# Optimization experiments

Measured on AMD Instinct MI355X. Metric: run time of the kernel, lower is better.

## Reference

```python
import jax, jax.numpy as jnp
import numpy as np

M = 0.25      # margin m
GAMMA = 64.0  # scale gamma
N, D = 8192, 128
NUM_CLASSES = 512


def setup_inputs() -> dict:
    key = jax.random.key(0)
    k1, k2 = jax.random.split(key)
    inputs = jax.random.normal(k1, (N, D), dtype=jnp.float32)
    targets = jax.random.randint(k2, (N,), 0, NUM_CLASSES, dtype=jnp.int64)
    return {"inputs": inputs, "targets": targets}


def reference(inputs, targets):
    # L2-normalize rows -> cosine similarity matrix [n, n]
    x = inputs / jnp.linalg.norm(inputs, axis=1, keepdims=True)
    sim = x @ x.T
    # positive mask: same label (includes diagonal, matching the torch code)
    mask = targets[:, None] == targets[None, :]

    Op, On = 1.0 + M, -M
    delta_p, delta_n = 1.0 - M, M

    sim_d = jax.lax.stop_gradient(sim)  # .detach() in torch
    ap = jnp.maximum(Op - sim_d, 0.0)
    an = jnp.maximum(sim_d + On, 0.0)

    logit_p = -ap * (sim - delta_p) * GAMMA
    logit_n = an * (sim - delta_n) * GAMMA

    neg_inf = jnp.float32(-jnp.inf)
    # per-row logsumexp over positives of -logit_p, over negatives of logit_n
    lp = jax.nn.logsumexp(jnp.where(mask, -logit_p, neg_inf), axis=1)
    ln = jax.nn.logsumexp(jnp.where(mask, neg_inf, logit_n), axis=1)

    return jnp.mean(jax.nn.softplus(ln + lp))
```

## Files before the change

kernel.cpp:

```cpp
#include <hip/hip_runtime.h>
#include <math.h>


#define NR    8192
#define DIMK  128
#define NT    64
#define NBLKS 512

typedef __attribute__((ext_vector_type(8))) short short8;
typedef __attribute__((ext_vector_type(4))) float f32x4;
typedef __attribute__((address_space(3))) uint32_t lds_u32;
typedef const __attribute__((address_space(1))) uint32_t glb_u32;

__device__ __forceinline__ unsigned short bf16_rne(float f) {
  uint32_t u = __float_as_uint(f);
  u += 0x7FFFu + ((u >> 16) & 1u);
  return (unsigned short)(u >> 16);
}


__global__ __launch_bounds__(256) void normalize_split_kernel(
    const float* __restrict__ x, unsigned short* __restrict__ xhi,
    unsigned short* __restrict__ xlo, float* __restrict__ gP,
    float* __restrict__ gN, int* __restrict__ counter) {
  if (blockIdx.x < 32)      gP[blockIdx.x * 256 + threadIdx.x] = 0.f;
  else if (blockIdx.x < 64) gN[(blockIdx.x - 32) * 256 + threadIdx.x] = 0.f;
  if (blockIdx.x == 64 && threadIdx.x == 0) *counter = 0;

  const int wave = threadIdx.x >> 6;
  const int lane = threadIdx.x & 63;
  const int row  = blockIdx.x * 4 + wave;
  const float2 v = ((const float2*)(x + (size_t)row * DIMK))[lane];
  float ss = v.x * v.x + v.y * v.y;
  #pragma unroll
  for (int s = 1; s < 64; s <<= 1) ss += __shfl_xor(ss, s);
  const float r = rsqrtf(ss);
  const float a = v.x * r, b = v.y * r;
  const unsigned short ha = bf16_rne(a), hb = bf16_rne(b);
  const float haf = __uint_as_float((uint32_t)ha << 16);
  const float hbf = __uint_as_float((uint32_t)hb << 16);
  ushort2 hi, lo;
  hi.x = ha; hi.y = hb;
  lo.x = bf16_rne(a - haf); lo.y = bf16_rne(b - hbf);
  ((ushort2*)xhi)[(size_t)row * 64 + lane] = hi;
  ((ushort2*)xlo)[(size_t)row * 64 + lane] = lo;
}

__global__ __launch_bounds__(512, 2) void simloss_kernel(
    const unsigned short* __restrict__ xhi, const unsigned short* __restrict__ xlo,
    const int* __restrict__ tgt, float* __restrict__ gP, float* __restrict__ gN,
    int* __restrict__ counter, float* __restrict__ out) {
  __shared__ unsigned short S[32768];
  __shared__ float colbuf[2][4][128][2];
  __shared__ int tAs[2][128];
  __shared__ int tBs[5][128];
  __shared__ float red[512];
  __shared__ int islast;

  const int tid  = threadIdx.x;
  const int wave = tid >> 6, lane = tid & 63;
  const int wy = wave & 3, wx = wave >> 2;
  const int q = lane >> 4, mcol = lane & 15;
  const bool isStage = (wy == 1) || (wy == 2);
  const bool isFlush = (wy == 0);
  const int srank = (wy - 1) + wx * 2;

  const int p  = blockIdx.x >> 4;
  const int b  = blockIdx.x & 15;
  const int n1 = NT - p;
  const int t0 = (b * (NT + 1)) >> 4;
  const int t1 = ((b + 1) * (NT + 1)) >> 4;
  const int ntile = t1 - t0;
  const int p2 = NT - 1 - p;

  int cur_bi = (t0 < n1) ? p : p2;

  if (tid < 128)       tAs[0][tid] = tgt[cur_bi * 128 + tid];
  else if (tid < 256)  tAs[1][tid - 128] = tgt[p2 * 128 + (tid - 128)];
  for (int v = tid; v < ntile * 128; v += 512) {
    const int ix = t0 + (v >> 7);
    const int bj = (ix < n1) ? p + ix : p2 + (ix - n1);
    tBs[v >> 7][v & 127] = tgt[bj * 128 + (v & 127)];
  }

  auto stageA = [&](int bi) {
    const unsigned short* gh = xhi + (size_t)bi * 128 * DIMK;
    const unsigned short* gl = xlo + (size_t)bi * 128 * DIMK;
    #pragma unroll
    for (int g = 0; g < 4; ++g) {
      const int r  = wave * 16 + g * 4 + (lane >> 4);
      const int sc = (lane & 15) ^ (r & 15);
      __builtin_amdgcn_global_load_lds((glb_u32*)(gh + (size_t)r * DIMK + sc * 8),
          (lds_u32*)&S[(wave * 16 + g * 4) * 128], 16, 0, 0);
      __builtin_amdgcn_global_load_lds((glb_u32*)(gl + (size_t)r * DIMK + sc * 8),
          (lds_u32*)&S[16384 + (wave * 16 + g * 4) * 128], 16, 0, 0);
    }
  };
  auto stageB = [&](int bj, int buf) {
    const unsigned short* gb = xhi + (size_t)bj * 128 * DIMK;
    unsigned short* dst = &S[buf * 16384];
    #pragma unroll
    for (int g = 0; g < 8; ++g) {
      const int r  = srank * 32 + g * 4 + (lane >> 4);
      const int sc = (lane & 15) ^ (r & 15);
      __builtin_amdgcn_global_load_lds((glb_u32*)(gb + (size_t)r * DIMK + sc * 8),
          (lds_u32*)&dst[(srank * 32 + g * 4) * 128], 16, 0, 0);
    }
  };

  short8 Ah[2][4], Al[2][4];
  int ta[2][4];
  auto extractA = [&](int seg) {
    #pragma unroll
    for (int fr = 0; fr < 2; ++fr) {
      const int r = wy * 32 + fr * 16 + mcol;
      #pragma unroll
      for (int ks = 0; ks < 4; ++ks) {
        const int pc = (ks * 4 + q) ^ mcol;
        Ah[fr][ks] = *(const short8*)&S[r * 128 + pc * 8];
        Al[fr][ks] = *(const short8*)&S[16384 + r * 128 + pc * 8];
      }
    }
    #pragma unroll
    for (int fr = 0; fr < 2; ++fr)
      #pragma unroll
      for (int rg = 0; rg < 4; ++rg)
        ta[fr][rg] = tAs[seg][wy * 32 + fr * 16 + q * 4 + rg];
  };

  float rowP[2][4] = {{0.f}}, rowN[2][4] = {{0.f}};
  auto flushRows = [&](int bi) {
    #pragma unroll
    for (int fr = 0; fr < 2; ++fr)
      #pragma unroll
      for (int rg = 0; rg < 4; ++rg) {
        float vp = rowP[fr][rg], vn = rowN[fr][rg];
        #pragma unroll
        for (int m = 1; m < 16; m <<= 1) {
          vp += __shfl_xor(vp, m);
          vn += __shfl_xor(vn, m);
        }
        if (mcol == 0) {
          const int row = bi * 128 + wy * 32 + fr * 16 + q * 4 + rg;
          atomicAdd(&gP[row], vp);
          atomicAdd(&gN[row], vn);
        }
      }
  };

  stageA(cur_bi);
  __syncthreads();
  extractA(0);
  __builtin_amdgcn_s_waitcnt(49279);
  __builtin_amdgcn_s_barrier();
  if (isStage) stageB((t0 < n1) ? p + t0 : p2 + (t0 - n1), 0);

  for (int tl = 0; tl < ntile; ++tl) {
    const int ix = t0 + tl;
    const int bi = (ix < n1) ? p : p2;
    const int bj = (ix < n1) ? p + ix : p2 + (ix - n1);

    if (bi != cur_bi) {
      flushRows(cur_bi);
      cur_bi = bi;
      stageA(cur_bi);
      __syncthreads();
      extractA(1);
      #pragma unroll
      for (int fr = 0; fr < 2; ++fr)
        #pragma unroll
        for (int rg = 0; rg < 4; ++rg) { rowP[fr][rg] = 0.f; rowN[fr][rg] = 0.f; }
      __builtin_amdgcn_s_waitcnt(49279);
      __builtin_amdgcn_s_barrier();
      if (isStage) stageB(bj, tl & 1);
    }

    if (isStage) __builtin_amdgcn_s_waitcnt(112);
    __builtin_amdgcn_s_barrier();

    if (tl + 1 < ntile) {
      const int ix2 = ix + 1;
      if ((ix2 < n1) == (ix < n1)) {
        const int bj2 = (ix2 < n1) ? p + ix2 : p2 + (ix2 - n1);
        if (isStage) stageB(bj2, (tl + 1) & 1);
      }
    }

    const unsigned short* Bb = &S[(tl & 1) * 16384];
    f32x4 acc[2][4];
    #pragma unroll
    for (int fr = 0; fr < 2; ++fr)
      #pragma unroll
      for (int fc = 0; fc < 4; ++fc)
        acc[fr][fc] = (f32x4){0.f, 0.f, 0.f, 0.f};
    #pragma unroll
    for (int ks = 0; ks < 4; ++ks) {
      short8 bh[4];
      #pragma unroll
      for (int fc = 0; fc < 4; ++fc) {
        const int rb = wx * 64 + fc * 16 + mcol;
        const int pc = (ks * 4 + q) ^ mcol;
        bh[fc] = *(const short8*)&Bb[rb * 128 + pc * 8];
      }
      #pragma unroll
      for (int fc = 0; fc < 4; ++fc) {
        acc[0][fc] = __builtin_amdgcn_mfma_f32_16x16x32_bf16(Ah[0][ks], bh[fc], acc[0][fc], 0, 0, 0);
        acc[1][fc] = __builtin_amdgcn_mfma_f32_16x16x32_bf16(Ah[1][ks], bh[fc], acc[1][fc], 0, 0, 0);
        acc[0][fc] = __builtin_amdgcn_mfma_f32_16x16x32_bf16(Al[0][ks], bh[fc], acc[0][fc], 0, 0, 0);
        acc[1][fc] = __builtin_amdgcn_mfma_f32_16x16x32_bf16(Al[1][ks], bh[fc], acc[1][fc], 0, 0, 0);
      }
    }

    int tb[4];
    #pragma unroll
    for (int fc = 0; fc < 4; ++fc) tb[fc] = tBs[tl][wx * 64 + fc * 16 + mcol];
    float cP[4] = {0.f, 0.f, 0.f, 0.f}, cN[4] = {0.f, 0.f, 0.f, 0.f};
    #pragma unroll
    for (int fr = 0; fr < 2; ++fr) {
      #pragma unroll
      for (int rg = 0; rg < 4; ++rg) {
        const int taa = ta[fr][rg];
        float vp = 0.f, vn = 0.f;
        #pragma unroll
        for (int fc = 0; fc < 4; ++fc) {
          const float s  = acc[fr][fc][rg];
          const bool pos = (taa == tb[fc]);
          const float ap = fmaxf(1.25f - s, 0.f);
          const float an = fmaxf(s - 0.25f, 0.f);
          const float arg = pos ? ap * fmaf(s, 64.f, -48.f) : an * an * 64.f;
          const float e = __expf(arg);
          const float ep = pos ? e : 0.f;
          const float en = pos ? 0.f : e;
          vp += ep; vn += en;
          cP[fc] += ep; cN[fc] += en;
        }
        rowP[fr][rg] += vp;
        rowN[fr][rg] += vn;
      }
    }

    #pragma unroll
    for (int fc = 0; fc < 4; ++fc) {
      cP[fc] += __shfl_xor(cP[fc], 16); cP[fc] += __shfl_xor(cP[fc], 32);
      cN[fc] += __shfl_xor(cN[fc], 16); cN[fc] += __shfl_xor(cN[fc], 32);
    }
    if (q == 0) {
      #pragma unroll
      for (int fc = 0; fc < 4; ++fc) {
        float2 v; v.x = cP[fc]; v.y = cN[fc];
        *(float2*)&colbuf[tl & 1][wy][wx * 64 + fc * 16 + mcol][0] = v;
      }
    }
    __builtin_amdgcn_s_waitcnt(49279);
    __builtin_amdgcn_s_barrier();

    if (isFlush && bj != bi) {
      const int col = wx * 64 + lane;
      float sp = 0.f, sn = 0.f;
      #pragma unroll
      for (int w = 0; w < 4; ++w) {
        const float2 v = *(const float2*)&colbuf[tl & 1][w][col][0];
        sp += v.x; sn += v.y;
      }
      atomicAdd(&gP[bj * 128 + col], sp);
      atomicAdd(&gN[bj * 128 + col], sn);
    }
  }
  flushRows(cur_bi);

  __builtin_amdgcn_s_waitcnt(0);
  __syncthreads();
  if (tid == 0) islast = (atomicAdd(counter, 1) == NBLKS - 1) ? 1 : 0;
  __syncthreads();
  if (islast) {
    float local = 0.f;
    #pragma unroll 1
    for (int bb = 0; bb < 2; ++bb) {
      const int base = bb * 4096 + tid * 8;
      float pv[8], nv[8];
      #pragma unroll
      for (int u = 0; u < 8; ++u) pv[u] = atomicAdd(&gP[base + u], 0.0f);
      #pragma unroll
      for (int u = 0; u < 8; ++u) nv[u] = atomicAdd(&gN[base + u], 0.0f);
      #pragma unroll
      for (int u = 0; u < 8; ++u) local += log1pf(pv[u] * nv[u]);
    }
    red[tid] = local;
    __syncthreads();
    for (int s2 = 256; s2 > 0; s2 >>= 1) {
      if (tid < s2) red[tid] += red[tid + s2];
      __syncthreads();
    }
    if (tid == 0) out[0] = red[0] / (float)NR;
  }
}

extern "C" void kernel_launch(void* const* d_in, const int* in_sizes, int n_in,
                              void* d_out, int out_size, void* d_ws, size_t ws_size,
                              hipStream_t stream) {
  const float* x  = (const float*)d_in[0];
  const int* tgt  = (const int*)d_in[1];
  float* out      = (float*)d_out;

  unsigned short* xhi = (unsigned short*)d_ws;
  unsigned short* xlo = xhi + (size_t)NR * DIMK;
  float* gP = (float*)((char*)d_ws + (size_t)NR * DIMK * 4);
  float* gN = gP + NR;
  int* counter = (int*)(gN + NR);

  normalize_split_kernel<<<NR / 4, 256, 0, stream>>>(x, xhi, xlo, gP, gN, counter);
  simloss_kernel<<<NBLKS, 512, 0, stream>>>(xhi, xlo, tgt, gP, gN, counter, out);
}
```

Baseline: 120.4 us.

## Treat all pairs as negatives and correct same-class pairs in a per-class pass

The main tiled loop now applies the negative-pair formula to every pair, with no label compares or selects. The exponent is rewritten as exp2 of a squared affine term using precomputed constants. The normalize kernel buckets row indices by class. Each block then handles one class: it computes that class's pairwise similarities in fp32, adds the positive terms and subtracts the negative terms that the main pass wrongly counted. This shrinks the per-element epilogue and drops the target staging, but adds a serial prologue, a memset launch, and a hard per-class cap (MAXC=120). Results are silently wrong if a class has more members than the cap, and the one-block-per-class mapping assumes the class count equals the block count.

```diff
diff --git a/kernel.cpp b/kernel.cpp
--- a/kernel.cpp
+++ b/kernel.cpp
@@ -6,6 +6,11 @@
 #define DIMK  128
 #define NT    64
 #define NBLKS 512
+#define NCLS  512
+#define MAXC  120
+
+#define CE1 9.6089795f
+#define CE0 -2.4022449f
 
 typedef __attribute__((ext_vector_type(8))) short short8;
 typedef __attribute__((ext_vector_type(4))) float f32x4;
@@ -18,11 +23,20 @@
   return (unsigned short)(u >> 16);
 }
 
+__device__ __forceinline__ float fexp2(float x) {
+#if __has_builtin(__builtin_amdgcn_exp2f)
+  return __builtin_amdgcn_exp2f(x);
+#else
+  return exp2f(x);
+#endif
+}
+
 
 __global__ __launch_bounds__(256) void normalize_split_kernel(
-    const float* __restrict__ x, unsigned short* __restrict__ xhi,
-    unsigned short* __restrict__ xlo, float* __restrict__ gP,
-    float* __restrict__ gN, int* __restrict__ counter) {
+    const float* __restrict__ x, const int* __restrict__ tgt,
+    unsigned short* __restrict__ xhi, unsigned short* __restrict__ xlo,
+    float* __restrict__ gP, float* __restrict__ gN,
+    int* __restrict__ cnt, int* __restrict__ idx, int* __restrict__ counter) {
   if (blockIdx.x < 32)      gP[blockIdx.x * 256 + threadIdx.x] = 0.f;
   else if (blockIdx.x < 64) gN[(blockIdx.x - 32) * 256 + threadIdx.x] = 0.f;
   if (blockIdx.x == 64 && threadIdx.x == 0) *counter = 0;
@@ -30,6 +44,13 @@
   const int wave = threadIdx.x >> 6;
   const int lane = threadIdx.x & 63;
   const int row  = blockIdx.x * 4 + wave;
+
+  if (lane == 0) {
+    const int t = tgt[row];
+    const int slot = atomicAdd(&cnt[t], 1);
+    if (slot < MAXC) idx[t * MAXC + slot] = row;
+  }
+
   const float2 v = ((const float2*)(x + (size_t)row * DIMK))[lane];
   float ss = v.x * v.x + v.y * v.y;
   #pragma unroll
@@ -48,13 +69,13 @@
 
 __global__ __launch_bounds__(512, 2) void simloss_kernel(
     const unsigned short* __restrict__ xhi, const unsigned short* __restrict__ xlo,
-    const int* __restrict__ tgt, float* __restrict__ gP, float* __restrict__ gN,
+    const int* __restrict__ cnt, const int* __restrict__ idx,
+    float* __restrict__ gP, float* __restrict__ gN,
     int* __restrict__ counter, float* __restrict__ out) {
   __shared__ unsigned short S[32768];
-  __shared__ float colbuf[2][4][128][2];
-  __shared__ int tAs[2][128];
-  __shared__ int tBs[5][128];
+  __shared__ float colbuf[2][4][128];
   __shared__ float red[512];
+  __shared__ int midx[MAXC];
   __shared__ int islast;
 
   const int tid  = threadIdx.x;
@@ -65,6 +86,38 @@
   const bool isFlush = (wy == 0);
   const int srank = (wy - 1) + wx * 2;
 
+  {
+    float* Sf = (float*)S;
+    const int cn = cnt[blockIdx.x];
+    const int m  = (cn < MAXC) ? cn : MAXC;
+    if (tid < m) midx[tid] = idx[blockIdx.x * MAXC + tid];
+    __syncthreads();
+    for (int v = tid; v < m * 128; v += 512) {
+      const int r = v >> 7, d = v & 127;
+      const int row = midx[r];
+      const float hi = __uint_as_float((uint32_t)xhi[(size_t)row * DIMK + d] << 16);
+      const float lo = __uint_as_float((uint32_t)xlo[(size_t)row * DIMK + d] << 16);
+      Sf[r * 129 + d] = hi + lo;
+    }
+    __syncthreads();
+    for (int pr = tid; pr < m * m; pr += 512) {
+      const int i = pr / m, j = pr - i * m;
+      const float* vi = &Sf[i * 129];
+      const float* vj = &Sf[j * 129];
+      float s = 0.f;
+      #pragma unroll 8
+      for (int d = 0; d < 128; ++d) s = fmaf(vi[d], vj[d], s);
+      const int gi = midx[i];
+      const float ep = __expf(fmaxf(1.25f - s, 0.f) * fmaf(s, 64.f, -48.f));
+      atomicAdd(&gP[gi], ep);
+      if (i != j) {
+        const float u = fmaxf(fmaf(s, CE1, CE0), 0.f);
+        atomicAdd(&gN[gi], -fexp2(u * u));
+      }
+    }
+    __syncthreads();
+  }
+
   const int p  = blockIdx.x >> 4;
   const int b  = blockIdx.x & 15;
   const int n1 = NT - p;
@@ -75,14 +128,6 @@
 
   int cur_bi = (t0 < n1) ? p : p2;
 
-  if (tid < 128)       tAs[0][tid] = tgt[cur_bi * 128 + tid];
-  else if (tid < 256)  tAs[1][tid - 128] = tgt[p2 * 128 + (tid - 128)];
-  for (int v = tid; v < ntile * 128; v += 512) {
-    const int ix = t0 + (v >> 7);
-    const int bj = (ix < n1) ? p + ix : p2 + (ix - n1);
-    tBs[v >> 7][v & 127] = tgt[bj * 128 + (v & 127)];
-  }
-
   auto stageA = [&](int bi) {
     const unsigned short* gh = xhi + (size_t)bi * 128 * DIMK;
     const unsigned short* gl = xlo + (size_t)bi * 128 * DIMK;
@@ -109,8 +154,7 @@
   };
 
   short8 Ah[2][4], Al[2][4];
-  int ta[2][4];
-  auto extractA = [&](int seg) {
+  auto extractA = [&]() {
     #pragma unroll
     for (int fr = 0; fr < 2; ++fr) {
       const int r = wy * 32 + fr * 16 + mcol;
@@ -121,36 +165,25 @@
         Al[fr][ks] = *(const short8*)&S[16384 + r * 128 + pc * 8];
       }
     }
+  };
+
+  float rowN[2][4] = {{0.f}};
+  auto flushRows = [&](int bi_) {
     #pragma unroll
     for (int fr = 0; fr < 2; ++fr)
       #pragma unroll
-      for (int rg = 0; rg < 4; ++rg)
-        ta[fr][rg] = tAs[seg][wy * 32 + fr * 16 + q * 4 + rg];
-  };
-
-  float rowP[2][4] = {{0.f}}, rowN[2][4] = {{0.f}};
-  auto flushRows = [&](int bi) {
-    #pragma unroll
-    for (int fr = 0; fr < 2; ++fr)
-      #pragma unroll
       for (int rg = 0; rg < 4; ++rg) {
-        float vp = rowP[fr][rg], vn = rowN[fr][rg];
+        float vn = rowN[fr][rg];
         #pragma unroll
-        for (int m = 1; m < 16; m <<= 1) {
-          vp += __shfl_xor(vp, m);
-          vn += __shfl_xor(vn, m);
-        }
-        if (mcol == 0) {
-          const int row = bi * 128 + wy * 32 + fr * 16 + q * 4 + rg;
-          atomicAdd(&gP[row], vp);
-          atomicAdd(&gN[row], vn);
-        }
+        for (int m2 = 1; m2 < 16; m2 <<= 1) vn += __shfl_xor(vn, m2);
+        if (mcol == 0)
+          atomicAdd(&gN[bi_ * 128 + wy * 32 + fr * 16 + q * 4 + rg], vn);
       }
   };
 
   stageA(cur_bi);
   __syncthreads();
-  extractA(0);
+  extractA();
   __builtin_amdgcn_s_waitcnt(49279);
   __builtin_amdgcn_s_barrier();
   if (isStage) stageB((t0 < n1) ? p + t0 : p2 + (t0 - n1), 0);
@@ -165,11 +198,11 @@
       cur_bi = bi;
       stageA(cur_bi);
       __syncthreads();
-      extractA(1);
+      extractA();
       #pragma unroll
       for (int fr = 0; fr < 2; ++fr)
         #pragma unroll
-        for (int rg = 0; rg < 4; ++rg) { rowP[fr][rg] = 0.f; rowN[fr][rg] = 0.f; }
+        for (int rg = 0; rg < 4; ++rg) rowN[fr][rg] = 0.f;
       __builtin_amdgcn_s_waitcnt(49279);
       __builtin_amdgcn_s_barrier();
       if (isStage) stageB(bj, tl & 1);
@@ -211,58 +244,52 @@
       }
     }
 
-    int tb[4];
-    #pragma unroll
-    for (int fc = 0; fc < 4; ++fc) tb[fc] = tBs[tl][wx * 64 + fc * 16 + mcol];
-    float cP[4] = {0.f, 0.f, 0.f, 0.f}, cN[4] = {0.f, 0.f, 0.f, 0.f};
-    #pragma unroll
-    for (int fr = 0; fr < 2; ++fr) {
-      #pragma unroll
-      for (int rg = 0; rg < 4; ++rg) {
-        const int taa = ta[fr][rg];
-        float vp = 0.f, vn = 0.f;
-        #pragma unroll
-        for (int fc = 0; fc < 4; ++fc) {
-          const float s  = acc[fr][fc][rg];
-          const bool pos = (taa == tb[fc]);
-          const float ap = fmaxf(1.25f - s, 0.f);
-          const float an = fmaxf(s - 0.25f, 0.f);
-          const float arg = pos ? ap * fmaf(s, 64.f, -48.f) : an * an * 64.f;
-          const float e = __expf(arg);
-          const float ep = pos ? e : 0.f;
-          const float en = pos ? 0.f : e;
-          vp += ep; vn += en;
-          cP[fc] += ep; cN[fc] += en;
-        }
-        rowP[fr][rg] += vp;
-        rowN[fr][rg] += vn;
-      }
-    }
+    float cN[4] = {0.f, 0.f, 0.f, 0.f};
+#define EPILOGUE(DIAG_)                                                      \
+    {                                                                        \
+      _Pragma("unroll")                                                      \
+      for (int fr = 0; fr < 2; ++fr) {                                       \
+        _Pragma("unroll")                                                    \
+        for (int rg = 0; rg < 4; ++rg) {                                     \
+          float vn = 0.f;                                                    \
+          _Pragma("unroll")                                                  \
+          for (int fc = 0; fc < 4; ++fc) {                                   \
+            const float s = acc[fr][fc][rg];                                 \
+            const float u = fmaxf(fmaf(s, CE1, CE0), 0.f);                   \
+            float e = fexp2(u * u);                                          \
+            if (DIAG_) {                                                     \
+              const int rl = wy * 32 + fr * 16 + q * 4 + rg;                 \
+              const int cl = wx * 64 + fc * 16 + mcol;                       \
+              e = (rl == cl) ? 0.f : e;                                      \
+            }                                                                \
+            vn += e;                                                         \
+            cN[fc] += e;                                                     \
+          }                                                                  \
+          rowN[fr][rg] += vn;                                                \
+        }                                                                    \
+      }                                                                      \
+    }
+    if (bj == bi) EPILOGUE(true) else EPILOGUE(false)
+#undef EPILOGUE
 
     #pragma unroll
     for (int fc = 0; fc < 4; ++fc) {
-      cP[fc] += __shfl_xor(cP[fc], 16); cP[fc] += __shfl_xor(cP[fc], 32);
-      cN[fc] += __shfl_xor(cN[fc], 16); cN[fc] += __shfl_xor(cN[fc], 32);
+      cN[fc] += __shfl_xor(cN[fc], 16);
+      cN[fc] += __shfl_xor(cN[fc], 32);
     }
     if (q == 0) {
       #pragma unroll
-      for (int fc = 0; fc < 4; ++fc) {
-        float2 v; v.x = cP[fc]; v.y = cN[fc];
-        *(float2*)&colbuf[tl & 1][wy][wx * 64 + fc * 16 + mcol][0] = v;
-      }
+      for (int fc = 0; fc < 4; ++fc)
+        colbuf[tl & 1][wy][wx * 64 + fc * 16 + mcol] = cN[fc];
     }
     __builtin_amdgcn_s_waitcnt(49279);
     __builtin_amdgcn_s_barrier();
 
     if (isFlush && bj != bi) {
       const int col = wx * 64 + lane;
-      float sp = 0.f, sn = 0.f;
-      #pragma unroll
-      for (int w = 0; w < 4; ++w) {
-        const float2 v = *(const float2*)&colbuf[tl & 1][w][col][0];
-        sp += v.x; sn += v.y;
-      }
-      atomicAdd(&gP[bj * 128 + col], sp);
+      float sn = 0.f;
+      #pragma unroll
+      for (int w = 0; w < 4; ++w) sn += colbuf[tl & 1][w][col];
       atomicAdd(&gN[bj * 128 + col], sn);
     }
   }
@@ -306,8 +333,11 @@
   unsigned short* xlo = xhi + (size_t)NR * DIMK;
   float* gP = (float*)((char*)d_ws + (size_t)NR * DIMK * 4);
   float* gN = gP + NR;
-  int* counter = (int*)(gN + NR);
-
-  normalize_split_kernel<<<NR / 4, 256, 0, stream>>>(x, xhi, xlo, gP, gN, counter);
-  simloss_kernel<<<NBLKS, 512, 0, stream>>>(xhi, xlo, tgt, gP, gN, counter, out);
-}
+  int* cnt = (int*)(gN + NR);
+  int* idx = cnt + NCLS;
+  int* counter = idx + NCLS * MAXC;
+
+  hipMemsetAsync(cnt, 0, NCLS * sizeof(int), stream);
+  normalize_split_kernel<<<NR / 4, 256, 0, stream>>>(x, tgt, xhi, xlo, gP, gN, cnt, idx, counter);
+  simloss_kernel<<<NBLKS, 512, 0, stream>>>(xhi, xlo, cnt, idx, gP, gN, counter, out);
+}
```

After: 124.4 us. +3.4%, slower.
